# Optimization experiments

Hardware: AMD Instinct MI355X
Metric: run time of the kernel (lower is better)

The kernel has to match this reference:

```python
import jax, jax.numpy as jnp
import numpy as np

EPS = 1e-5

def _bn(x, p):
    # p: (4, C) rows = gamma, beta, running_mean, running_var ; x: (B, C, H, W)
    g, b, m, v = p[0], p[1], p[2], p[3]
    sh = (1, -1, 1, 1)
    return (x - m.reshape(sh)) * (g.reshape(sh) * jax.lax.rsqrt(v.reshape(sh) + EPS)) + b.reshape(sh)

def _cba1(x, w, p):
    # 1x1 conv (no bias) + BN + ReLU
    return jax.nn.relu(_bn(jnp.einsum('oc,bchw->bohw', w, x), p))

def setup_inputs() -> dict:
    B, C, H, W = 2, 512, 128, 256
    CK, K, CO = 256, 19, 512
    key = jax.random.key(0)
    ks = jax.random.split(key, 10)
    def w(k, shape, fan):
        return jax.random.normal(k, shape, jnp.float32) * (fan ** -0.5)
    def bn(c):
        return jnp.stack([jnp.ones((c,), jnp.float32), jnp.zeros((c,), jnp.float32),
                          jnp.zeros((c,), jnp.float32), jnp.ones((c,), jnp.float32)])
    return {
        'x': jax.random.normal(ks[0], (B, C, H, W), jnp.float32),
        'proxy_feats': jax.random.normal(ks[1], (B, C, K, 1), jnp.float32),
        'wq1': w(ks[2], (CK, C), C),  'bnq1': bn(CK),
        'wq2': w(ks[3], (CK, CK), CK), 'bnq2': bn(CK),
        'wk1': w(ks[4], (CK, C), C),  'bnk1': bn(CK),
        'wk2': w(ks[5], (CK, CK), CK), 'bnk2': bn(CK),
        'wv':  w(ks[6], (CK, C), C),  'bnv':  bn(CK),
        'wout': w(ks[7], (C, CK), CK), 'bnout': bn(C),
        'wbot': w(ks[8], (CO, 2 * C, 3, 3), 2 * C * 9), 'bnbot': bn(CO),
    }

def reference(x, proxy_feats, wq1, wq2, wk1, wk2, wv, wout, wbot,
              bnq1, bnq2, bnk1, bnk2, bnv, bnout, bnbot):
    B, C, H, W = x.shape
    CK = wq1.shape[0]
    # --- ObjectContextBlock: pixel-region cross attention ---
    q = _cba1(_cba1(x, wq1, bnq1), wq2, bnq2)            # (B, CK, H, W)
    k = _cba1(_cba1(proxy_feats, wk1, bnk1), wk2, bnk2)  # (B, CK, K, 1)
    v = _cba1(proxy_feats, wv, bnv)                      # (B, CK, K, 1)
    q = q.reshape(B, CK, H * W)                          # (B, CK, N)
    k = k.reshape(B, CK, -1)                             # (B, CK, K)
    v = v.reshape(B, CK, -1)                             # (B, CK, K)
    sim = jnp.einsum('bcn,bck->bnk', q, k) * (CK ** -0.5)
    sim = jax.nn.softmax(sim, axis=-1)                   # (B, N, K)
    ctx = jnp.einsum('bnk,bck->bcn', sim, v).reshape(B, CK, H, W)
    ctx = _cba1(ctx, wout, bnout)                        # (B, C, H, W)
    # --- bottleneck: concat + 3x3 conv + BN + ReLU ---
    cat = jnp.concatenate([ctx, x], axis=1)              # (B, 2C, H, W)
    out = jax.lax.conv_general_dilated(cat, wbot, (1, 1), 'SAME',
                                       dimension_numbers=('NCHW', 'OIHW', 'NCHW'))
    return jax.nn.relu(_bn(out, bnbot))
```

## Files before the change

### kernel.cpp

```cpp
#include <hip/hip_runtime.h>
#include <cstdint>

#define EPS 1e-5f
#define PADW 258
#define PADROWS 33540
#define NPIX 32768

typedef __attribute__((ext_vector_type(8))) short bf16x8;
typedef __attribute__((ext_vector_type(4))) float f32x4;

__device__ __forceinline__ ushort f2bf(float f) {
  union { float f; uint32_t u; } v; v.f = f;
  uint32_t r = v.u + 0x7fffu + ((v.u >> 16) & 1u);
  return (ushort)(r >> 16);
}
__device__ __forceinline__ float bf2f(ushort h) {
  union { uint32_t u; float f; } v; v.u = ((uint32_t)h) << 16;
  return v.f;
}
__device__ __forceinline__ void gload_lds16(const void* g, void* lds) {
  __builtin_amdgcn_global_load_lds((__attribute__((address_space(1))) void*)g,
                                   (__attribute__((address_space(3))) void*)lds,
                                   16, 0, 0);
}

template <int BMODE, int OMODE>
__global__ __launch_bounds__(256) void mfma_gemm(
    const ushort* __restrict__ A, const ushort* __restrict__ B,
    const float* __restrict__ bn, void* __restrict__ OutV,
    int M, int K, int pitchB, int ciB, long strideB, int pitchO, long strideO) {
  const int lane = threadIdx.x & 63;
  const int wave = threadIdx.x >> 6;
  const int wm = (wave & 1) * 64;
  const int wn = (wave >> 1) * 64;
  const int m0 = blockIdx.y * 128;
  const int n0 = blockIdx.x * 128;
  const int z  = blockIdx.z;
  B += (size_t)z * strideB;

  const int h = n0 >> 8, w0 = n0 & 255;
  long prowB;
  if (BMODE == 0) prowB = n0;
  else            prowB = (long)(h + 1) * PADW + (w0 + 1);

  __shared__ __align__(16) ushort Asl[4 * 128 * 8];
  __shared__ __align__(16) ushort Bsl[4 * 128 * 8];

  f32x4 acc[4][4];
#pragma unroll
  for (int mt = 0; mt < 4; ++mt)
#pragma unroll
    for (int nt = 0; nt < 4; ++nt) acc[mt][nt] = (f32x4){0.f, 0.f, 0.f, 0.f};

  for (int k0 = 0; k0 < K; k0 += 32) {
#pragma unroll
    for (int i = 0; i < 2; ++i) {
      int s = wave * 2 + i;
      int c = s * 64 + lane;
      int mm = c & 127, ks = c >> 7;
      gload_lds16(A + (size_t)(m0 + mm) * K + (k0 + ks * 8), Asl + s * 512);
    }
    long rowb; int cib;
    if (BMODE == 2) {
      int tap = k0 >> 10;
      int dy = tap / 3 - 1, dx = tap % 3 - 1;
      rowb = prowB + dy * PADW + dx;
      cib  = k0 & 1023;
    } else {
      rowb = prowB;
      cib  = ciB + k0;
    }
#pragma unroll
    for (int i = 0; i < 2; ++i) {
      int s = wave * 2 + i;
      int c = s * 64 + lane;
      int nn = c & 127, ks = c >> 7;
      gload_lds16(B + (size_t)(rowb + nn) * pitchB + cib + ks * 8, Bsl + s * 512);
    }
    __syncthreads();
    bf16x8 af[4], bfr[4];
#pragma unroll
    for (int t = 0; t < 4; ++t) {
      af[t]  = *(const bf16x8*)(Asl + (((lane >> 4) * 128) + wm + t * 16 + (lane & 15)) * 8);
      bfr[t] = *(const bf16x8*)(Bsl + (((lane >> 4) * 128) + wn + t * 16 + (lane & 15)) * 8);
    }
#pragma unroll
    for (int mt = 0; mt < 4; ++mt)
#pragma unroll
      for (int nt = 0; nt < 4; ++nt)
        acc[mt][nt] = __builtin_amdgcn_mfma_f32_16x16x32_bf16(af[mt], bfr[nt], acc[mt][nt], 0, 0, 0);
    __syncthreads();
  }

  const int q4 = lane >> 4, col = lane & 15;
  float scv[16], bov[16];
#pragma unroll
  for (int mt = 0; mt < 4; ++mt)
#pragma unroll
    for (int r = 0; r < 4; ++r) {
      int m = m0 + wm + mt * 16 + q4 * 4 + r;
      float s = bn[m] * rsqrtf(bn[3 * M + m] + EPS);
      scv[mt * 4 + r] = s;
      bov[mt * 4 + r] = bn[M + m] - bn[2 * M + m] * s;
    }
  if (OMODE == 2) {
    float* Outf = (float*)OutV + (size_t)z * strideO;
#pragma unroll
    for (int mt = 0; mt < 4; ++mt)
#pragma unroll
      for (int r = 0; r < 4; ++r) {
        int m = m0 + wm + mt * 16 + q4 * 4 + r;
        float* rowp = Outf + (size_t)m * NPIX + n0 + wn;
#pragma unroll
        for (int nt = 0; nt < 4; ++nt)
          rowp[nt * 16 + col] = fmaxf(acc[mt][nt][r] * scv[mt * 4 + r] + bov[mt * 4 + r], 0.f);
      }
  } else {
    ushort* Outh = (ushort*)OutV + (size_t)z * strideO;
    long prowO = (OMODE == 0) ? (long)n0 : ((long)(h + 1) * PADW + (w0 + 1));
#pragma unroll
    for (int nt = 0; nt < 4; ++nt) {
      long row = prowO + wn + nt * 16 + col;
      ushort* p = Outh + (size_t)row * pitchO + m0 + wm;
#pragma unroll
      for (int mt = 0; mt < 4; ++mt) {
        ushort4 pk;
        pk.x = f2bf(fmaxf(acc[mt][nt][0] * scv[mt * 4 + 0] + bov[mt * 4 + 0], 0.f));
        pk.y = f2bf(fmaxf(acc[mt][nt][1] * scv[mt * 4 + 1] + bov[mt * 4 + 1], 0.f));
        pk.z = f2bf(fmaxf(acc[mt][nt][2] * scv[mt * 4 + 2] + bov[mt * 4 + 2], 0.f));
        pk.w = f2bf(fmaxf(acc[mt][nt][3] * scv[mt * 4 + 3] + bov[mt * 4 + 3], 0.f));
        *(ushort4*)(p + mt * 16 + q4 * 4) = pk;
      }
    }
  }
}

#define PXS  130
#define ROWC (PXS * 4)
#define BUFC (3 * ROWC)
__global__ __launch_bounds__(256, 3) void conv3x3_mfma(
    const ushort* __restrict__ W2, const ushort* __restrict__ cat,
    const float* __restrict__ bn, float* __restrict__ out) {
  const int tid  = threadIdx.x;
  const int lane = tid & 63;
  const int wave = tid >> 6;
  const int wm = (wave & 1) * 64;
  const int wn = (wave >> 1) * 64;
  const int m0 = (blockIdx.x & 3) * 128;
  const int n0 = (blockIdx.x >> 2) * 128;
  const int z  = blockIdx.z;
  const int h = n0 >> 8, w0 = n0 & 255;
  const long prow0 = (long)(h + 1) * PADW + (w0 + 1);
  const ushort* Bz = cat + (size_t)z * PADROWS * 1024;

  __shared__ __align__(16) ushort halo[2 * BUFC * 8];

  f32x4 acc[4][4];
#pragma unroll
  for (int mt = 0; mt < 4; ++mt)
#pragma unroll
    for (int nt = 0; nt < 4; ++nt) acc[mt][nt] = (f32x4){0.f, 0.f, 0.f, 0.f};

  long offs[7];
#pragma unroll
  for (int s = 0; s < 7; ++s) {
    int c = s * 256 + tid;
    if (c < BUFC) {
      int o_slot = c & 3;
      int q = c >> 2;
      int p = q % PXS;
      int r = q / PXS;
      int o_g = o_slot ^ ((p >> 1) & 3);
      offs[s] = ((prow0 + (long)(r - 1) * PADW + (p - 1)) << 10) + o_g * 8;
    } else {
      offs[s] = -1;
    }
  }

  auto stage = [&](int buf, int ci0n) {
#pragma unroll
    for (int s = 0; s < 7; ++s)
      if (offs[s] >= 0)
        gload_lds16(Bz + offs[s] + ci0n,
                    halo + ((size_t)buf * BUFC + s * 256 + wave * 64) * 8);
  };

  const ushort* Alane = W2 + (size_t)(m0 + wm + (lane & 15)) * 32 + (lane >> 4) * 8;

  const int p0  = wn + (lane & 15);
  const int oct = lane >> 4;
  int hoff[12];
#pragma unroll
  for (int nt = 0; nt < 4; ++nt)
#pragma unroll
    for (int dx = 0; dx < 3; ++dx) {
      int p = p0 + nt * 16 + dx;
      hoff[nt * 3 + dx] = (p * 4 + (oct ^ ((p >> 1) & 3))) * 16;
    }

  stage(0, 0);
  __syncthreads();

  for (int it = 0; it < 32; ++it) {
    const ushort* Ait = Alane + (size_t)it * (9 * 16384);

    bf16x8 af[3][4];
#pragma unroll
    for (int t = 0; t < 3; ++t)
#pragma unroll
      for (int mt = 0; mt < 4; ++mt)
        af[t][mt] = *(const bf16x8*)(Ait + (size_t)t * 16384 + mt * 512);

    __builtin_amdgcn_sched_barrier(0);
    if (it < 31) stage((it + 1) & 1, (it + 1) * 32);
    __builtin_amdgcn_sched_barrier(0);

    const char* hb0 = (const char*)(halo + (size_t)(it & 1) * BUFC * 8);
#pragma unroll
    for (int t = 0; t < 9; ++t) {
      const int slot = t % 3;
      const int r = t / 3, dx = t % 3;
      bf16x8 bfr[4];
#pragma unroll
      for (int nt = 0; nt < 4; ++nt)
        bfr[nt] = *(const bf16x8*)(hb0 + r * (ROWC * 16) + hoff[nt * 3 + dx]);
      __builtin_amdgcn_s_setprio(1);
#pragma unroll
      for (int nt = 0; nt < 4; ++nt)
#pragma unroll
        for (int mt = 0; mt < 4; ++mt)
          acc[mt][nt] = __builtin_amdgcn_mfma_f32_16x16x32_bf16(af[slot][mt], bfr[nt], acc[mt][nt], 0, 0, 0);
      __builtin_amdgcn_s_setprio(0);
      if (t < 6) {
#pragma unroll
        for (int mt = 0; mt < 4; ++mt)
          af[slot][mt] = *(const bf16x8*)(Ait + (size_t)(t + 3) * 16384 + mt * 512);
      }
    }
    __syncthreads();
  }

  const int q4 = lane >> 4, col = lane & 15;
  float* Outf = out + (size_t)z * 512 * NPIX;
#pragma unroll
  for (int mt = 0; mt < 4; ++mt)
#pragma unroll
    for (int r = 0; r < 4; ++r) {
      int m = m0 + wm + mt * 16 + q4 * 4 + r;
      float s  = bn[m] * rsqrtf(bn[3 * 512 + m] + EPS);
      float bo = bn[512 + m] - bn[2 * 512 + m] * s;
      float* rowp = Outf + (size_t)m * NPIX + n0 + wn;
#pragma unroll
      for (int nt = 0; nt < 4; ++nt)
        rowp[nt * 16 + col] = fmaxf(acc[mt][nt][r] * s + bo, 0.f);
    }
}

__global__ __launch_bounds__(64) void small_gemm_kernel(
    const float* __restrict__ Wm, const float* __restrict__ X,
    const float* __restrict__ bn, float* __restrict__ Y,
    int CO, int CI, int KC) {
  int co = blockIdx.x, b = blockIdx.y, kc = threadIdx.x;
  if (kc >= KC) return;
  const float* Xb = X + (size_t)b * CI * KC;
  float acc = 0.f;
  for (int c = 0; c < CI; ++c) acc += Wm[(size_t)co * CI + c] * Xb[(size_t)c * KC + kc];
  float s  = bn[co] * rsqrtf(bn[3 * CO + co] + EPS);
  float bs = bn[CO + co] - bn[2 * CO + co] * s;
  Y[((size_t)b * CO + co) * KC + kc] = fmaxf(acc * s + bs, 0.f);
}

__global__ __launch_bounds__(256) void attention_kernel(
    const ushort* __restrict__ qT, const float* __restrict__ Kp,
    const float* __restrict__ Vp, ushort* __restrict__ ctxT) {
  int b = blockIdx.y;
  int pix = blockIdx.x * 256 + threadIdx.x;
  __shared__ float ks[256][19], vs[256][19];
  for (int idx = threadIdx.x; idx < 256 * 19; idx += 256) {
    int c = idx / 19, kk = idx % 19;
    ks[c][kk] = Kp[((size_t)b * 256 + c) * 19 + kk];
    vs[c][kk] = Vp[((size_t)b * 256 + c) * 19 + kk];
  }
  __syncthreads();

  const ushort* qrow = qT + ((size_t)b * NPIX + pix) * 256;
  float sim[19];
#pragma unroll
  for (int kk = 0; kk < 19; ++kk) sim[kk] = 0.f;
  for (int c0 = 0; c0 < 256; c0 += 8) {
    uint4 raw = *(const uint4*)(qrow + c0);
    float qf[8] = {bf2f((ushort)(raw.x & 0xffff)), bf2f((ushort)(raw.x >> 16)),
                   bf2f((ushort)(raw.y & 0xffff)), bf2f((ushort)(raw.y >> 16)),
                   bf2f((ushort)(raw.z & 0xffff)), bf2f((ushort)(raw.z >> 16)),
                   bf2f((ushort)(raw.w & 0xffff)), bf2f((ushort)(raw.w >> 16))};
#pragma unroll
    for (int j = 0; j < 8; ++j)
#pragma unroll
      for (int kk = 0; kk < 19; ++kk) sim[kk] += qf[j] * ks[c0 + j][kk];
  }
  const float scale = 0.0625f;
  float mx = -1e30f;
#pragma unroll
  for (int kk = 0; kk < 19; ++kk) { sim[kk] *= scale; mx = fmaxf(mx, sim[kk]); }
  float denom = 0.f;
#pragma unroll
  for (int kk = 0; kk < 19; ++kk) { sim[kk] = __expf(sim[kk] - mx); denom += sim[kk]; }
  float inv = 1.f / denom;
#pragma unroll
  for (int kk = 0; kk < 19; ++kk) sim[kk] *= inv;

  ushort* crow = ctxT + ((size_t)b * NPIX + pix) * 256;
  for (int c0 = 0; c0 < 256; c0 += 8) {
    uint32_t o[4];
#pragma unroll
    for (int j = 0; j < 4; ++j) {
      float v0 = 0.f, v1 = 0.f;
#pragma unroll
      for (int kk = 0; kk < 19; ++kk) {
        v0 += sim[kk] * vs[c0 + j * 2][kk];
        v1 += sim[kk] * vs[c0 + j * 2 + 1][kk];
      }
      o[j] = (uint32_t)f2bf(v0) | ((uint32_t)f2bf(v1) << 16);
    }
    *(uint4*)(crow + c0) = make_uint4(o[0], o[1], o[2], o[3]);
  }
}

__global__ __launch_bounds__(256) void transpose_x_kernel(
    const float* __restrict__ x, ushort* __restrict__ cat) {
  int b = blockIdx.z, ci0 = blockIdx.y * 64, n0 = blockIdx.x * 64;
  __shared__ float t[64][65];
  const float* xb = x + ((size_t)b * 512 + ci0) * NPIX + n0;
  for (int i = 0; i < 16; ++i) {
    int idx = i * 256 + threadIdx.x;
    int c = idx >> 6, w = idx & 63;
    t[c][w] = xb[(size_t)c * NPIX + w];
  }
  __syncthreads();
  int h = n0 >> 8, w0 = n0 & 255;
  size_t pbase = ((size_t)b * PADROWS + (size_t)(h + 1) * PADW + (w0 + 1)) * 1024 + 512 + ci0;
  for (int i = 0; i < 16; ++i) {
    int idx = i * 256 + threadIdx.x;
    int n = idx >> 6, c = idx & 63;
    cat[pbase + (size_t)n * 1024 + c] = f2bf(t[c][n]);
  }
}

__global__ void convert_w_kernel(const float* __restrict__ in, ushort* __restrict__ out, int n) {
  int i = blockIdx.x * 256 + threadIdx.x;
  if (i < n) out[i] = f2bf(in[i]);
}
__global__ void repack_conv_w_kernel(const float* __restrict__ wbot, ushort* __restrict__ Wrb) {
  int idx = blockIdx.x * 256 + threadIdx.x;
  if (idx >= 512 * 9216) return;
  int ci_in = idx & 31;
  int r  = idx >> 5;
  int co = r & 511;
  int tt = r >> 9;
  int t = tt % 9, chunk = tt / 9;
  Wrb[idx] = f2bf(wbot[((size_t)co * 1024 + chunk * 32 + ci_in) * 9 + t]);
}

extern "C" void kernel_launch(void* const* d_in, const int* in_sizes, int n_in,
                              void* d_out, int out_size, void* d_ws, size_t ws_size,
                              hipStream_t stream) {
  const float* x     = (const float*)d_in[0];
  const float* proxy = (const float*)d_in[1];
  const float* wq1   = (const float*)d_in[2];
  const float* bnq1  = (const float*)d_in[3];
  const float* wq2   = (const float*)d_in[4];
  const float* bnq2  = (const float*)d_in[5];
  const float* wk1   = (const float*)d_in[6];
  const float* bnk1  = (const float*)d_in[7];
  const float* wk2   = (const float*)d_in[8];
  const float* bnk2  = (const float*)d_in[9];
  const float* wv    = (const float*)d_in[10];
  const float* bnv   = (const float*)d_in[11];
  const float* wout  = (const float*)d_in[12];
  const float* bnout = (const float*)d_in[13];
  const float* wbot  = (const float*)d_in[14];
  const float* bnbot = (const float*)d_in[15];
  float* out = (float*)d_out;

  const int B = 2, C = 512, CK = 256, KC = 19;
  char* ws = (char*)d_ws;
  const size_t catBytes = (size_t)B * PADROWS * 1024 * 2;
  ushort* cat  = (ushort*)ws;
  ushort* bufA = (ushort*)(ws + 137379840);
  ushort* bufB = (ushort*)(ws + 137379840 + 33554432);
  ushort* Wrb  = (ushort*)(ws + 204488704);
  ushort* wq1b = (ushort*)(ws + 213925888);
  ushort* wq2b = (ushort*)(ws + 214188032);
  ushort* woutb= (ushort*)(ws + 214319104);
  float*  k1   = (float*)(ws + 214581248);
  float*  k2   = k1 + (size_t)B * CK * KC;
  float*  vv   = k2 + (size_t)B * CK * KC;

  hipMemsetAsync(cat, 0, catBytes, stream);

  convert_w_kernel<<<(CK * C + 255) / 256, 256, 0, stream>>>(wq1, wq1b, CK * C);
  convert_w_kernel<<<(CK * CK + 255) / 256, 256, 0, stream>>>(wq2, wq2b, CK * CK);
  convert_w_kernel<<<(C * CK + 255) / 256, 256, 0, stream>>>(wout, woutb, C * CK);
  repack_conv_w_kernel<<<(512 * 9216 + 255) / 256, 256, 0, stream>>>(wbot, Wrb);

  small_gemm_kernel<<<dim3(CK, B), 64, 0, stream>>>(wk1, proxy, bnk1, k1, CK, C, KC);
  small_gemm_kernel<<<dim3(CK, B), 64, 0, stream>>>(wk2, k1, bnk2, k2, CK, CK, KC);
  small_gemm_kernel<<<dim3(CK, B), 64, 0, stream>>>(wv, proxy, bnv, vv, CK, C, KC);

  transpose_x_kernel<<<dim3(NPIX / 64, 8, B), 256, 0, stream>>>(x, cat);

  const long padStride = (long)PADROWS * 1024;
  const long nckStride = (long)NPIX * 256;

  mfma_gemm<1, 0><<<dim3(NPIX / 128, 2, B), 256, 0, stream>>>(
      wq1b, cat, bnq1, bufA, 256, 512, 1024, 512, padStride, 256, nckStride);
  mfma_gemm<0, 0><<<dim3(NPIX / 128, 2, B), 256, 0, stream>>>(
      wq2b, bufA, bnq2, bufB, 256, 256, 256, 0, nckStride, 256, nckStride);

  attention_kernel<<<dim3(NPIX / 256, B), 256, 0, stream>>>(bufB, k2, vv, bufA);

  mfma_gemm<0, 1><<<dim3(NPIX / 128, 4, B), 256, 0, stream>>>(
      woutb, bufA, bnout, cat, 512, 256, 256, 0, nckStride, 1024, padStride);

  conv3x3_mfma<<<dim3((NPIX / 128) * 4, 1, B), 256, 0, stream>>>(Wrb, cat, bnbot, out);
}
```

Before: 1.300 ms.

## Swizzle GEMM LDS layout and software-pipeline conv weight and halo loads

The 1x1 GEMM kernel now stores A and B tiles in LDS with an XOR-swizzled k-group layout, to cut bank conflicts on the MFMA fragment reads. The 3x3 conv kernel now prefetches the next iteration's first three weight taps during the current iteration, double-buffers the halo fragment reads one tap ahead, and replaces __syncthreads with a partial vmcnt wait plus s_barrier so outstanding weight loads can stay in flight. The hand-counted vmcnt(12) is fragile: if the compiler issues a different number or order of loads, the barrier could pass before the staged LDS data has landed. The extra prefetch buffers also raise register pressure.

```diff
diff --git a/kernel.cpp b/kernel.cpp
--- a/kernel.cpp
+++ b/kernel.cpp
@@ -55,10 +55,9 @@
   for (int k0 = 0; k0 < K; k0 += 32) {
 #pragma unroll
     for (int i = 0; i < 2; ++i) {
-      int s = wave * 2 + i;
-      int c = s * 64 + lane;
-      int mm = c & 127, ks = c >> 7;
-      gload_lds16(A + (size_t)(m0 + mm) * K + (k0 + ks * 8), Asl + s * 512);
+      int c = (wave * 2 + i) * 64 + lane;
+      int mm = c >> 2, g = (c & 3) ^ ((mm >> 1) & 3);
+      gload_lds16(A + (size_t)(m0 + mm) * K + (k0 + g * 8), Asl + c * 8);
     }
     long rowb; int cib;
     if (BMODE == 2) {
@@ -72,17 +71,19 @@
     }
 #pragma unroll
     for (int i = 0; i < 2; ++i) {
-      int s = wave * 2 + i;
-      int c = s * 64 + lane;
-      int nn = c & 127, ks = c >> 7;
-      gload_lds16(B + (size_t)(rowb + nn) * pitchB + cib + ks * 8, Bsl + s * 512);
+      int c = (wave * 2 + i) * 64 + lane;
+      int nn = c >> 2, g = (c & 3) ^ ((nn >> 1) & 3);
+      gload_lds16(B + (size_t)(rowb + nn) * pitchB + cib + g * 8, Bsl + c * 8);
     }
     __syncthreads();
     bf16x8 af[4], bfr[4];
 #pragma unroll
     for (int t = 0; t < 4; ++t) {
-      af[t]  = *(const bf16x8*)(Asl + (((lane >> 4) * 128) + wm + t * 16 + (lane & 15)) * 8);
-      bfr[t] = *(const bf16x8*)(Bsl + (((lane >> 4) * 128) + wn + t * 16 + (lane & 15)) * 8);
+      int ks = lane >> 4;
+      int ma = wm + t * 16 + (lane & 15);
+      int nb = wn + t * 16 + (lane & 15);
+      af[t]  = *(const bf16x8*)(Asl + (ma * 4 + (ks ^ ((ma >> 1) & 3))) * 8);
+      bfr[t] = *(const bf16x8*)(Bsl + (nb * 4 + (ks ^ ((nb >> 1) & 3))) * 8);
     }
 #pragma unroll
     for (int mt = 0; mt < 4; ++mt)
@@ -199,45 +200,60 @@
     }
 
   stage(0, 0);
-  __syncthreads();
+  bf16x8 af[3][4];
+#pragma unroll
+  for (int t = 0; t < 3; ++t)
+#pragma unroll
+    for (int mt = 0; mt < 4; ++mt)
+      af[t][mt] = *(const bf16x8*)(Alane + (size_t)t * 16384 + mt * 512);
+
+  asm volatile("s_waitcnt vmcnt(12)" ::: "memory");
+  __builtin_amdgcn_sched_barrier(0);
+  __builtin_amdgcn_s_barrier();
+  __builtin_amdgcn_sched_barrier(0);
 
   for (int it = 0; it < 32; ++it) {
     const ushort* Ait = Alane + (size_t)it * (9 * 16384);
-
-    bf16x8 af[3][4];
-#pragma unroll
-    for (int t = 0; t < 3; ++t)
-#pragma unroll
-      for (int mt = 0; mt < 4; ++mt)
-        af[t][mt] = *(const bf16x8*)(Ait + (size_t)t * 16384 + mt * 512);
-
-    __builtin_amdgcn_sched_barrier(0);
+    const ushort* An  = (it < 31) ? Ait + (size_t)(9 * 16384) : Ait;
     if (it < 31) stage((it + 1) & 1, (it + 1) * 32);
     __builtin_amdgcn_sched_barrier(0);
 
     const char* hb0 = (const char*)(halo + (size_t)(it & 1) * BUFC * 8);
+    bf16x8 bfr[2][4];
+#pragma unroll
+    for (int nt = 0; nt < 4; ++nt)
+      bfr[0][nt] = *(const bf16x8*)(hb0 + hoff[nt * 3]);
+
 #pragma unroll
     for (int t = 0; t < 9; ++t) {
       const int slot = t % 3;
-      const int r = t / 3, dx = t % 3;
-      bf16x8 bfr[4];
+      if (t < 8) {
+        const int r = (t + 1) / 3, dx = (t + 1) % 3;
+#pragma unroll
+        for (int nt = 0; nt < 4; ++nt)
+          bfr[(t + 1) & 1][nt] = *(const bf16x8*)(hb0 + r * (ROWC * 16) + hoff[nt * 3 + dx]);
+      }
+      __builtin_amdgcn_s_setprio(1);
 #pragma unroll
       for (int nt = 0; nt < 4; ++nt)
-        bfr[nt] = *(const bf16x8*)(hb0 + r * (ROWC * 16) + hoff[nt * 3 + dx]);
-      __builtin_amdgcn_s_setprio(1);
-#pragma unroll
-      for (int nt = 0; nt < 4; ++nt)
 #pragma unroll
         for (int mt = 0; mt < 4; ++mt)
-          acc[mt][nt] = __builtin_amdgcn_mfma_f32_16x16x32_bf16(af[slot][mt], bfr[nt], acc[mt][nt], 0, 0, 0);
+          acc[mt][nt] = __builtin_amdgcn_mfma_f32_16x16x32_bf16(af[slot][mt], bfr[t & 1][nt], acc[mt][nt], 0, 0, 0);
       __builtin_amdgcn_s_setprio(0);
       if (t < 6) {
 #pragma unroll
         for (int mt = 0; mt < 4; ++mt)
           af[slot][mt] = *(const bf16x8*)(Ait + (size_t)(t + 3) * 16384 + mt * 512);
+      } else {
+#pragma unroll
+        for (int mt = 0; mt < 4; ++mt)
+          af[slot][mt] = *(const bf16x8*)(An + (size_t)(t - 6) * 16384 + mt * 512);
       }
     }
-    __syncthreads();
+    asm volatile("s_waitcnt vmcnt(12)" ::: "memory");
+    __builtin_amdgcn_sched_barrier(0);
+    __builtin_amdgcn_s_barrier();
+    __builtin_amdgcn_sched_barrier(0);
   }
 
   const int q4 = lane >> 4, col = lane & 15;
```

Result: slower. 1.379 ms (+6.1%).
